# Kernel tuning notes

Measured on AMD Instinct MI355X. Metric: run time of the kernel, lower is better.

The kernel has to match this reference:

```python
import jax, jax.numpy as jnp
import numpy as np

N_NODES = 100000
D_IN = 128
H_DIM = 128
N_EDGES = 1600000


def _gcn_conv(x, src, dst, dinv, W, b):
    # PyG GCNConv(improved=True): h = x @ W; out = A_hat h + b,
    # A_hat = D^{-1/2} (A + 2I) D^{-1/2}
    h = x @ W                                   # [N, H]
    norm = dinv[src] * dinv[dst]                # [E]
    agg = jnp.zeros_like(h).at[dst].add(h[src] * norm[:, None])
    agg = agg + h * (2.0 * dinv * dinv)[:, None]  # self-loop, weight 2.0
    return agg + b


def setup_inputs() -> dict:
    key = jax.random.key(0)
    ks = jax.random.split(key, 12)
    s = 1.0 / np.sqrt(D_IN)
    sh = 1.0 / np.sqrt(2 * H_DIM)
    inp = {
        "x": jax.random.normal(ks[0], (N_NODES, D_IN), jnp.float32),
        "edge_index": jax.random.randint(ks[1], (2, N_EDGES), 0, N_NODES, jnp.int64),
        # GCNConv weights (in -> hidden), bias
        "Wz": jax.random.uniform(ks[2], (D_IN, H_DIM), jnp.float32, -s, s),
        "bz": jnp.zeros((H_DIM,), jnp.float32),
        "Wr": jax.random.uniform(ks[3], (D_IN, H_DIM), jnp.float32, -s, s),
        "br": jnp.zeros((H_DIM,), jnp.float32),
        "Wh": jax.random.uniform(ks[4], (D_IN, H_DIM), jnp.float32, -s, s),
        "bh": jnp.zeros((H_DIM,), jnp.float32),
        # TGCN gate linears: Linear(2h, h)
        "lzW": jax.random.uniform(ks[5], (2 * H_DIM, H_DIM), jnp.float32, -sh, sh),
        "lzb": jax.random.uniform(ks[6], (H_DIM,), jnp.float32, -sh, sh),
        "lrW": jax.random.uniform(ks[7], (2 * H_DIM, H_DIM), jnp.float32, -sh, sh),
        "lrb": jax.random.uniform(ks[8], (H_DIM,), jnp.float32, -sh, sh),
        "lhW": jax.random.uniform(ks[9], (2 * H_DIM, H_DIM), jnp.float32, -sh, sh),
        "lhb": jax.random.uniform(ks[10], (H_DIM,), jnp.float32, -sh, sh),
        # final linear2: hidden -> 1
        "W2": jax.random.uniform(ks[11], (H_DIM, 1), jnp.float32, -1 / np.sqrt(H_DIM), 1 / np.sqrt(H_DIM)),
        "b2": jnp.zeros((1,), jnp.float32),
    }
    return inp


def reference(x, edge_index, Wz, bz, Wr, br, Wh, bh, lzW, lzb, lrW, lrb, lhW, lhb, W2, b2):
    src, dst = edge_index[0], edge_index[1]
    n = x.shape[0]
    # improved GCN norm: deg includes self-loop weight 2
    deg = jnp.zeros((n,), x.dtype).at[dst].add(jnp.ones_like(src, x.dtype)) + 2.0
    dinv = jnp.where(deg > 0, deg ** -0.5, 0.0)
    # TGCN cell with H0 = 0
    H0 = jnp.zeros((n, Wz.shape[1]), x.dtype)
    Z = jax.nn.sigmoid(jnp.concatenate([_gcn_conv(x, src, dst, dinv, Wz, bz), H0], axis=1) @ lzW + lzb)
    R = jax.nn.sigmoid(jnp.concatenate([_gcn_conv(x, src, dst, dinv, Wr, br), H0], axis=1) @ lrW + lrb)
    Ht = jnp.tanh(jnp.concatenate([_gcn_conv(x, src, dst, dinv, Wh, bh), H0 * R], axis=1) @ lhW + lhb)
    H = Z * H0 + (1.0 - Z) * Ht
    # forward: relu output is discarded (y = h overwrites), then linear2
    return H @ W2 + b2
```

## Files before the change

### kernel.cpp

```cpp
#include <hip/hip_runtime.h>
#include <math.h>

#define D 128
#define BSHIFT 9
#define NB 196
#define EPT 7
#define P1B 241
#define CAPB 80
#define PSTRIDE (P1B * CAPB)
#define ECAP 9216
#define XCB4 782
#define PRB 32

typedef __attribute__((ext_vector_type(8))) short s8v;
typedef __attribute__((ext_vector_type(8))) unsigned short us8;
typedef __attribute__((ext_vector_type(4))) unsigned short us4;
typedef __attribute__((ext_vector_type(4))) float f4v;

__device__ __forceinline__ float bf2f(unsigned short u) {
    union { unsigned int i; float f; } v; v.i = ((unsigned int)u) << 16; return v.f;
}
__device__ __forceinline__ unsigned short f2bf(float f) {
    union { float f; unsigned int i; } v; v.f = f;
    unsigned int r = v.i + 0x7FFFu + ((v.i >> 16) & 1u);
    return (unsigned short)(r >> 16);
}

__global__ __launch_bounds__(1024) void k_pre(
    const int* __restrict__ src, const int* __restrict__ dst, int E,
    unsigned int* __restrict__ pairs, int* __restrict__ runlen,
    const float* __restrict__ x, unsigned short* __restrict__ xb, int n4,
    const float* __restrict__ Wz, const float* __restrict__ bz,
    const float* __restrict__ lzW, const float* __restrict__ lzb,
    const float* __restrict__ Wh, const float* __restrict__ bh,
    const float* __restrict__ lhW, const float* __restrict__ lhb,
    unsigned short* __restrict__ Mt, float* __restrict__ c) {
    __shared__ int cnt[256];
    __shared__ int loff[256];
    __shared__ unsigned int stage[EPT * 1024];
    int bx = blockIdx.x, tid = threadIdx.x;

    if (bx < P1B) {
        unsigned int pk[EPT]; int rkbk[EPT];
        int e0 = bx * (EPT * 1024) + tid;
        if (tid < 256) cnt[tid] = 0;
        __syncthreads();
        #pragma unroll
        for (int i = 0; i < EPT; ++i) {
            int e = e0 + i * 1024;
            bool ok = e < E;
            int d = ok ? dst[e] : 0;
            int s = ok ? src[e] : 0;
            int bk = d >> BSHIFT;
            pk[i] = ((unsigned int)(d & ((1 << BSHIFT) - 1)) << 17) | (unsigned int)s;
            int r = ok ? atomicAdd(&cnt[bk], 1) : 0;
            rkbk[i] = ok ? ((bk << 16) | r) : -1;
        }
        __syncthreads();
        if (tid < 64) {
            int v0 = cnt[tid * 4], v1 = cnt[tid * 4 + 1], v2 = cnt[tid * 4 + 2], v3 = cnt[tid * 4 + 3];
            int s = v0 + v1 + v2 + v3;
            int sc = s;
            #pragma unroll
            for (int off = 1; off < 64; off <<= 1) {
                int o = __shfl_up(sc, off, 64);
                if (tid >= off) sc += o;
            }
            int excl = sc - s;
            loff[tid * 4]     = excl;
            loff[tid * 4 + 1] = excl + v0;
            loff[tid * 4 + 2] = excl + v0 + v1;
            loff[tid * 4 + 3] = excl + v0 + v1 + v2;
        }
        __syncthreads();
        #pragma unroll
        for (int i = 0; i < EPT; ++i) {
            if (rkbk[i] >= 0) {
                int bk = rkbk[i] >> 16;
                stage[loff[bk] + (rkbk[i] & 0xffff)] = pk[i];
            }
        }
        if (tid < 256) runlen[bx * 256 + tid] = cnt[tid];
        __syncthreads();
        int wv = tid >> 6, lane = tid & 63;
        for (int b = wv; b < 256; b += 16) {
            int len = cnt[b];
            if (len == 0) continue;
            int lo = loff[b];
            unsigned int gbase = (unsigned int)b * PSTRIDE + (unsigned int)bx * CAPB;
            for (int j = lane; j < len; j += 64)
                pairs[gbase + j] = stage[lo + j];
        }
    } else if (bx < P1B + XCB4) {
        int i0 = (bx - P1B) * 4096 + tid;
        #pragma unroll
        for (int u = 0; u < 4; ++u) {
            int i = i0 + u * 1024;
            if (i < n4) {
                float4 v = ((const float4*)x)[i];
                us4 o;
                o[0] = f2bf(v.x); o[1] = f2bf(v.y); o[2] = f2bf(v.z); o[3] = f2bf(v.w);
                ((us4*)xb)[i] = o;
            }
        }
    } else {
        int k = (bx - (P1B + XCB4)) * 4 + (tid >> 8);
        int j = tid & 255;
        int jj = j & 127;
        const float* W = (j < 128) ? Wz : Wh;
        const float* L = (j < 128) ? lzW : lhW;
        float s = 0.f;
        for (int t = 0; t < 128; ++t) s += W[k * 128 + t] * L[t * 128 + jj];
        Mt[(size_t)j * 128 + k] = f2bf(s);
        if (k == 0) {
            const float* b  = (j < 128) ? bz  : bh;
            const float* lb = (j < 128) ? lzb : lhb;
            float cs = lb[jj];
            for (int t = 0; t < 128; ++t) cs += b[t] * L[t * 128 + jj];
            c[j] = cs;
        }
    }
}

__global__ __launch_bounds__(1024) void k_part2(
    const unsigned int* __restrict__ pairs, const int* __restrict__ runlen,
    int N,
    int* __restrict__ rowptr, int* __restrict__ deg, float* __restrict__ dinv,
    int* __restrict__ esrc) {
    __shared__ int cnt2[512];
    __shared__ int lcur[512];
    __shared__ int rl[256];
    __shared__ int sstage[ECAP];
    __shared__ int stot;
    int b = blockIdx.x, tid = threadIdx.x;
    int n0 = b << BSHIFT;
    int nn = min(N - n0, 1 << BSHIFT);
    long pb = (long)b * PSTRIDE;
    int wv = tid >> 6, lane = tid & 63;

    if (tid < 256) rl[tid] = (tid < P1B) ? runlen[tid * 256 + b] : 0;
    if (tid < 512) cnt2[tid] = 0;
    __syncthreads();
    for (int r = wv; r < P1B; r += 16) {
        int len = rl[r];
        long rb = pb + r * CAPB;
        for (int j = lane; j < len; j += 64)
            atomicAdd(&cnt2[pairs[rb + j] >> 17], 1);
    }
    __syncthreads();
    if (tid < 64) {
        int v[8]; int s = 0;
        #pragma unroll
        for (int k = 0; k < 8; ++k) { v[k] = cnt2[tid * 8 + k]; s += v[k]; }
        int sc = s;
        #pragma unroll
        for (int off = 1; off < 64; off <<= 1) {
            int o = __shfl_up(sc, off, 64);
            if (tid >= off) sc += o;
        }
        int excl = sc - s;
        if (tid == 63) stot = sc;
        #pragma unroll
        for (int k = 0; k < 8; ++k) {
            int node = tid * 8 + k;
            lcur[node] = excl;
            if (node < nn) {
                rowptr[n0 + node] = b * ECAP + excl;
                deg[n0 + node]    = v[k];
                dinv[n0 + node]   = rsqrtf((float)v[k] + 2.0f);
            }
            excl += v[k];
        }
    }
    __syncthreads();
    for (int r = wv; r < P1B; r += 16) {
        int len = rl[r];
        long rb = pb + r * CAPB;
        for (int j = lane; j < len; j += 64) {
            unsigned int p = pairs[rb + j];
            int pos = atomicAdd(&lcur[p >> 17], 1);
            sstage[pos] = (int)(p & 0x1FFFFu);
        }
    }
    __syncthreads();
    int tot = stot;
    for (int i = tid; i < tot; i += 1024)
        esrc[b * ECAP + i] = sstage[i];
}

__global__ __launch_bounds__(256) void k_gather(const unsigned short* __restrict__ xb,
                                                const int* __restrict__ esrc,
                                                const int* __restrict__ rowptr,
                                                const int* __restrict__ deg,
                                                const float* __restrict__ dinv,
                                                unsigned short* __restrict__ xab, int N) {
    int node = (blockIdx.x * blockDim.x + threadIdx.x) >> 5;
    int sub  = threadIdx.x & 31;
    if (node >= N) return;
    int eo = sub >> 4, cs = sub & 15;
    int start = rowptr[node];
    int end = start + deg[node];
    float dd = dinv[node];
    float acc[8];
    #pragma unroll
    for (int j = 0; j < 8; ++j) acc[j] = 0.f;

    for (int base = start; base < end; base += 32) {
        int cnt = min(32, end - base);
        int myedge = 0; float mynorm = 0.f;
        if (sub < cnt) { myedge = esrc[base + sub]; mynorm = dinv[myedge]; }
        int pairs = (cnt + 1) >> 1;
        int i = 0;
        for (; i + 3 < pairs; i += 4) {
            int i0 = 2 * i + eo;
            int   s0 = __shfl(myedge, i0,     32); float w0 = __shfl(mynorm, i0,     32);
            int   s1 = __shfl(myedge, i0 + 2, 32); float w1 = __shfl(mynorm, i0 + 2, 32);
            int   s2 = __shfl(myedge, i0 + 4, 32); float w2 = __shfl(mynorm, i0 + 4, 32);
            int   s3 = __shfl(myedge, i0 + 6, 32); float w3 = __shfl(mynorm, i0 + 6, 32);
            us8 v0 = *(const us8*)(xb + (size_t)s0 * D + cs * 8);
            us8 v1 = *(const us8*)(xb + (size_t)s1 * D + cs * 8);
            us8 v2 = *(const us8*)(xb + (size_t)s2 * D + cs * 8);
            us8 v3 = *(const us8*)(xb + (size_t)s3 * D + cs * 8);
            #pragma unroll
            for (int j = 0; j < 8; ++j) acc[j] += bf2f(v0[j]) * w0;
            #pragma unroll
            for (int j = 0; j < 8; ++j) acc[j] += bf2f(v1[j]) * w1;
            #pragma unroll
            for (int j = 0; j < 8; ++j) acc[j] += bf2f(v2[j]) * w2;
            #pragma unroll
            for (int j = 0; j < 8; ++j) acc[j] += bf2f(v3[j]) * w3;
        }
        for (; i < pairs; ++i) {
            int i0 = 2 * i + eo;
            int   s0 = __shfl(myedge, i0, 32); float w0 = __shfl(mynorm, i0, 32);
            us8 v0 = *(const us8*)(xb + (size_t)s0 * D + cs * 8);
            #pragma unroll
            for (int j = 0; j < 8; ++j) acc[j] += bf2f(v0[j]) * w0;
        }
    }
    #pragma unroll
    for (int j = 0; j < 8; ++j) acc[j] += __shfl_xor(acc[j], 16);
    if (eo == 0) {
        us8 xs = *(const us8*)(xb + (size_t)node * D + cs * 8);
        float sfac = 2.f * dd * dd;
        us8 r;
        #pragma unroll
        for (int j = 0; j < 8; ++j) r[j] = f2bf(acc[j] * dd + bf2f(xs[j]) * sfac);
        *(us8*)(xab + (size_t)node * D + cs * 8) = r;
    }
}

#define ASTRIDE 136
__global__ __launch_bounds__(256, 4) void k_ep_mfma(
    const unsigned short* __restrict__ xab, const unsigned short* __restrict__ Mt,
    const float* __restrict__ c, const float* __restrict__ W2,
    const float* __restrict__ b2, float* __restrict__ out, int N) {
    __shared__ unsigned short Ast[64 * ASTRIDE];
    __shared__ float pbuf[4][64];

    int tid = threadIdx.x;
    int n0 = blockIdx.x * 64;
    int wv = tid >> 6;
    int lane = tid & 63;
    int l = lane & 15, q = lane >> 4;

    #pragma unroll
    for (int j = 0; j < 4; ++j) {
        int idx = tid + 256 * j;
        int row = idx >> 4, c16 = idx & 15;
        us8 v = {0, 0, 0, 0, 0, 0, 0, 0};
        if (n0 + row < N) v = *(const us8*)(xab + (size_t)(n0 + row) * D + c16 * 8);
        *(us8*)&Ast[row * ASTRIDE + c16 * 8] = v;
    }
    __syncthreads();

    int tz0 = 2 * wv;
    f4v acc[4][4];
    #pragma unroll
    for (int i = 0; i < 4; ++i)
        #pragma unroll
        for (int nt = 0; nt < 4; ++nt) acc[i][nt] = (f4v){0.f, 0.f, 0.f, 0.f};

    const unsigned short* Bb = Mt + (size_t)l * 128 + q * 8;

    #pragma unroll
    for (int ks = 0; ks < 4; ++ks) {
        s8v b[4];
        #pragma unroll
        for (int i = 0; i < 2; ++i) {
            b[i]     = *(const s8v*)(Bb + (size_t)(tz0 + i) * 16 * 128 + ks * 32);
            b[2 + i] = *(const s8v*)(Bb + (size_t)(8 + tz0 + i) * 16 * 128 + ks * 32);
        }
        #pragma unroll
        for (int nt = 0; nt < 4; ++nt) {
            s8v a = *(const s8v*)&Ast[(nt * 16 + l) * ASTRIDE + ks * 32 + q * 8];
            #pragma unroll
            for (int i = 0; i < 4; ++i)
                acc[i][nt] = __builtin_amdgcn_mfma_f32_16x16x32_bf16(a, b[i], acc[i][nt], 0, 0, 0);
        }
    }

    float p[4][4];
    #pragma unroll
    for (int nt = 0; nt < 4; ++nt)
        #pragma unroll
        for (int r = 0; r < 4; ++r) p[nt][r] = 0.f;
    #pragma unroll
    for (int i = 0; i < 2; ++i) {
        int col = (tz0 + i) * 16 + l;
        float cz = c[col], ch = c[128 + col], w2 = W2[col];
        #pragma unroll
        for (int nt = 0; nt < 4; ++nt)
            #pragma unroll
            for (int r = 0; r < 4; ++r) {
                float gz = acc[i][nt][r] + cz;
                float gh = acc[2 + i][nt][r] + ch;
                float z  = 1.f / (1.f + __expf(-gz));
                float ht = 1.f - 2.f / (__expf(2.f * gh) + 1.f);
                p[nt][r] += (1.f - z) * ht * w2;
            }
    }
    #pragma unroll
    for (int nt = 0; nt < 4; ++nt)
        #pragma unroll
        for (int r = 0; r < 4; ++r) {
            p[nt][r] += __shfl_xor(p[nt][r], 1);
            p[nt][r] += __shfl_xor(p[nt][r], 2);
            p[nt][r] += __shfl_xor(p[nt][r], 4);
            p[nt][r] += __shfl_xor(p[nt][r], 8);
        }
    if (l == 0) {
        #pragma unroll
        for (int nt = 0; nt < 4; ++nt)
            #pragma unroll
            for (int r = 0; r < 4; ++r)
                pbuf[wv][nt * 16 + q * 4 + r] = p[nt][r];
    }
    __syncthreads();
    if (tid < 64) {
        int n = n0 + tid;
        if (n < N)
            out[n] = pbuf[0][tid] + pbuf[1][tid] + pbuf[2][tid] + pbuf[3][tid] + b2[0];
    }
}

extern "C" void kernel_launch(void* const* d_in, const int* in_sizes, int n_in,
                              void* d_out, int out_size, void* d_ws, size_t ws_size,
                              hipStream_t stream) {
    const float* x    = (const float*)d_in[0];
    const int*   eidx = (const int*)d_in[1];
    const float* Wz   = (const float*)d_in[2];
    const float* bz   = (const float*)d_in[3];
    const float* Wh   = (const float*)d_in[6];
    const float* bh   = (const float*)d_in[7];
    const float* lzW  = (const float*)d_in[8];
    const float* lzb  = (const float*)d_in[9];
    const float* lhW  = (const float*)d_in[12];
    const float* lhb  = (const float*)d_in[13];
    const float* W2   = (const float*)d_in[14];
    const float* b2   = (const float*)d_in[15];
    float* out = (float*)d_out;

    int N = in_sizes[0] / D;
    int E = in_sizes[1] / 2;
    const int* src = eidx;
    const int* dst = eidx + E;

    char* ws = (char*)d_ws;
    size_t off = 0;
    auto alloc = [&](size_t bytes) { void* p = ws + off; off += (bytes + 511) & ~(size_t)511; return p; };
    unsigned short* xb  = (unsigned short*)alloc((size_t)N * D * 2);
    unsigned short* xab = (unsigned short*)alloc((size_t)N * D * 2);
    int*   rowptr = (int*)  alloc((size_t)N * 4);
    int*   deg    = (int*)  alloc((size_t)N * 4);
    float* dinv   = (float*)alloc((size_t)N * 4);
    int*   esrc   = (int*)  alloc((size_t)NB * ECAP * 4);
    int*   runlen = (int*)  alloc((size_t)P1B * 256 * 4);
    unsigned short* Mt = (unsigned short*)alloc(256 * 128 * 2);
    float* c      = (float*)alloc(256 * 4);
    unsigned int* pairs = (unsigned int*)xab;

    int n4 = N * (D / 4);
    k_pre<<<P1B + XCB4 + PRB, 1024, 0, stream>>>(
        src, dst, E, pairs, runlen,
        x, xb, n4, Wz, bz, lzW, lzb, Wh, bh, lhW, lhb, Mt, c);
    k_part2<<<NB, 1024, 0, stream>>>(pairs, runlen, N, rowptr, deg, dinv, esrc);
    k_gather<<<(N * 32 + 255) / 256, 256, 0, stream>>>(xb, esrc, rowptr, deg, dinv, xab, N);
    k_ep_mfma<<<(N + 63) / 64, 256, 0, stream>>>(xab, Mt, c, W2, b2, out, N);
}
```

Measured before the change: 231.4 us.

## Compact bucket pair storage with global atomic cursors instead of fixed-capacity runs

Each first-pass block now reserves space in its destination bucket through a per-bucket global atomicAdd, so pairs are stored contiguously in a buffer of ECAP entries per bucket rather than in fixed 80-slot runs per source block. The second pass then reads one dense range per bucket with every thread striding over it, instead of walking 241 variable-length runs wave by wave. This removes the run-length array and the underused, poorly balanced loops over runs. It adds a memset and global atomics, and it makes the order of edges within a bucket nondeterministic.

```diff
diff --git a/kernel.cpp b/kernel.cpp
--- a/kernel.cpp
+++ b/kernel.cpp
@@ -6,8 +6,6 @@
 #define NB 196
 #define EPT 7
 #define P1B 241
-#define CAPB 80
-#define PSTRIDE (P1B * CAPB)
 #define ECAP 9216
 #define XCB4 782
 #define PRB 32
@@ -28,7 +26,7 @@
 
 __global__ __launch_bounds__(1024) void k_pre(
     const int* __restrict__ src, const int* __restrict__ dst, int E,
-    unsigned int* __restrict__ pairs, int* __restrict__ runlen,
+    unsigned int* __restrict__ pairs, int* __restrict__ gcur,
     const float* __restrict__ x, unsigned short* __restrict__ xb, int n4,
     const float* __restrict__ Wz, const float* __restrict__ bz,
     const float* __restrict__ lzW, const float* __restrict__ lzb,
@@ -80,14 +78,16 @@
                 stage[loff[bk] + (rkbk[i] & 0xffff)] = pk[i];
             }
         }
-        if (tid < 256) runlen[bx * 256 + tid] = cnt[tid];
         __syncthreads();
         int wv = tid >> 6, lane = tid & 63;
         for (int b = wv; b < 256; b += 16) {
             int len = cnt[b];
             if (len == 0) continue;
             int lo = loff[b];
-            unsigned int gbase = (unsigned int)b * PSTRIDE + (unsigned int)bx * CAPB;
+            int base = 0;
+            if (lane == 0) base = atomicAdd(&gcur[b], len);
+            base = __shfl(base, 0, 64);
+            unsigned int gbase = (unsigned int)b * ECAP + (unsigned int)base;
             for (int j = lane; j < len; j += 64)
                 pairs[gbase + j] = stage[lo + j];
         }
@@ -123,30 +123,23 @@
 }
 
 __global__ __launch_bounds__(1024) void k_part2(
-    const unsigned int* __restrict__ pairs, const int* __restrict__ runlen,
+    const unsigned int* __restrict__ pairs, const int* __restrict__ gcur,
     int N,
     int* __restrict__ rowptr, int* __restrict__ deg, float* __restrict__ dinv,
     int* __restrict__ esrc) {
     __shared__ int cnt2[512];
     __shared__ int lcur[512];
-    __shared__ int rl[256];
     __shared__ int sstage[ECAP];
-    __shared__ int stot;
     int b = blockIdx.x, tid = threadIdx.x;
     int n0 = b << BSHIFT;
     int nn = min(N - n0, 1 << BSHIFT);
-    long pb = (long)b * PSTRIDE;
-    int wv = tid >> 6, lane = tid & 63;
-
-    if (tid < 256) rl[tid] = (tid < P1B) ? runlen[tid * 256 + b] : 0;
+    int tot = gcur[b];
+    unsigned int bb = (unsigned int)b * ECAP;
+
     if (tid < 512) cnt2[tid] = 0;
     __syncthreads();
-    for (int r = wv; r < P1B; r += 16) {
-        int len = rl[r];
-        long rb = pb + r * CAPB;
-        for (int j = lane; j < len; j += 64)
-            atomicAdd(&cnt2[pairs[rb + j] >> 17], 1);
-    }
+    for (int j = tid; j < tot; j += 1024)
+        atomicAdd(&cnt2[pairs[bb + j] >> 17], 1);
     __syncthreads();
     if (tid < 64) {
         int v[8]; int s = 0;
@@ -159,7 +152,6 @@
             if (tid >= off) sc += o;
         }
         int excl = sc - s;
-        if (tid == 63) stot = sc;
         #pragma unroll
         for (int k = 0; k < 8; ++k) {
             int node = tid * 8 + k;
@@ -173,19 +165,14 @@
         }
     }
     __syncthreads();
-    for (int r = wv; r < P1B; r += 16) {
-        int len = rl[r];
-        long rb = pb + r * CAPB;
-        for (int j = lane; j < len; j += 64) {
-            unsigned int p = pairs[rb + j];
-            int pos = atomicAdd(&lcur[p >> 17], 1);
-            sstage[pos] = (int)(p & 0x1FFFFu);
-        }
-    }
-    __syncthreads();
-    int tot = stot;
+    for (int j = tid; j < tot; j += 1024) {
+        unsigned int p = pairs[bb + j];
+        int pos = atomicAdd(&lcur[p >> 17], 1);
+        sstage[pos] = (int)(p & 0x1FFFFu);
+    }
+    __syncthreads();
     for (int i = tid; i < tot; i += 1024)
-        esrc[b * ECAP + i] = sstage[i];
+        esrc[bb + i] = sstage[i];
 }
 
 __global__ __launch_bounds__(256) void k_gather(const unsigned short* __restrict__ xb,
@@ -375,16 +362,17 @@
     int*   deg    = (int*)  alloc((size_t)N * 4);
     float* dinv   = (float*)alloc((size_t)N * 4);
     int*   esrc   = (int*)  alloc((size_t)NB * ECAP * 4);
-    int*   runlen = (int*)  alloc((size_t)P1B * 256 * 4);
     unsigned short* Mt = (unsigned short*)alloc(256 * 128 * 2);
     float* c      = (float*)alloc(256 * 4);
+    int*   gcur   = (int*)  alloc(256 * 4);
     unsigned int* pairs = (unsigned int*)xab;
 
     int n4 = N * (D / 4);
+    hipMemsetAsync(gcur, 0, 256 * sizeof(int), stream);
     k_pre<<<P1B + XCB4 + PRB, 1024, 0, stream>>>(
-        src, dst, E, pairs, runlen,
+        src, dst, E, pairs, gcur,
         x, xb, n4, Wz, bz, lzW, lzb, Wh, bh, lhW, lhb, Mt, c);
-    k_part2<<<NB, 1024, 0, stream>>>(pairs, runlen, N, rowptr, deg, dinv, esrc);
+    k_part2<<<NB, 1024, 0, stream>>>(pairs, gcur, N, rowptr, deg, dinv, esrc);
     k_gather<<<(N * 32 + 255) / 256, 256, 0, stream>>>(xb, esrc, rowptr, deg, dinv, xab, N);
     k_ep_mfma<<<(N + 63) / 64, 256, 0, stream>>>(xab, Mt, c, W2, b2, out, N);
 }
```

Result: slower. 403.2 us (+74.2%).

## Regroup preprocessing kernels, cache pairs in LDS, and double-tile the epilogue

Applied to the files above, without the earlier changes.

The x-to-bf16 conversion and the weight-folding blocks move out of the edge-partition kernel and into the second-stage kernel. They now run alongside the per-bucket CSR build instead of alongside the first edge pass. The second stage reads pairs from global memory once into an LDS raw buffer and does its scatter from LDS, where before it read global memory twice. Part1 writes pairs as uint2 pairs. The MFMA epilogue now handles two 64-row tiles per block and prefetches the second tile's rows into registers while the first is being computed. This is meant to hide load latency, at the cost of more registers and more LDS use, which can lower occupancy.

```diff
diff --git a/kernel.cpp b/kernel.cpp
--- a/kernel.cpp
+++ b/kernel.cpp
@@ -26,39 +26,102 @@
     return (unsigned short)(r >> 16);
 }
 
-__global__ __launch_bounds__(1024) void k_pre(
+__global__ __launch_bounds__(1024) void k_part1(
     const int* __restrict__ src, const int* __restrict__ dst, int E,
-    unsigned int* __restrict__ pairs, int* __restrict__ runlen,
+    unsigned int* __restrict__ pairs, int* __restrict__ runlen) {
+    __shared__ int cnt[256];
+    __shared__ int loff[256];
+    __shared__ unsigned int stage[EPT * 1024];
+    int bx = blockIdx.x, tid = threadIdx.x;
+
+    unsigned int pk[EPT]; int rkbk[EPT];
+    int e0 = bx * (EPT * 1024) + tid;
+    if (tid < 256) cnt[tid] = 0;
+    __syncthreads();
+    #pragma unroll
+    for (int i = 0; i < EPT; ++i) {
+        int e = e0 + i * 1024;
+        bool ok = e < E;
+        int d = ok ? dst[e] : 0;
+        int s = ok ? src[e] : 0;
+        int bk = d >> BSHIFT;
+        pk[i] = ((unsigned int)(d & ((1 << BSHIFT) - 1)) << 17) | (unsigned int)s;
+        int r = ok ? atomicAdd(&cnt[bk], 1) : 0;
+        rkbk[i] = ok ? ((bk << 16) | r) : -1;
+    }
+    __syncthreads();
+    if (tid < 64) {
+        int v0 = cnt[tid * 4], v1 = cnt[tid * 4 + 1], v2 = cnt[tid * 4 + 2], v3 = cnt[tid * 4 + 3];
+        int s = v0 + v1 + v2 + v3;
+        int sc = s;
+        #pragma unroll
+        for (int off = 1; off < 64; off <<= 1) {
+            int o = __shfl_up(sc, off, 64);
+            if (tid >= off) sc += o;
+        }
+        int excl = sc - s;
+        loff[tid * 4]     = excl;
+        loff[tid * 4 + 1] = excl + v0;
+        loff[tid * 4 + 2] = excl + v0 + v1;
+        loff[tid * 4 + 3] = excl + v0 + v1 + v2;
+    }
+    __syncthreads();
+    #pragma unroll
+    for (int i = 0; i < EPT; ++i) {
+        if (rkbk[i] >= 0) {
+            int bk = rkbk[i] >> 16;
+            stage[loff[bk] + (rkbk[i] & 0xffff)] = pk[i];
+        }
+    }
+    if (tid < 256) runlen[bx * 256 + tid] = cnt[tid];
+    __syncthreads();
+    int wv = tid >> 6, lane = tid & 63;
+    for (int b = wv; b < 256; b += 16) {
+        int len = cnt[b];
+        if (len == 0) continue;
+        int lo = loff[b];
+        unsigned int gbase = (unsigned int)b * PSTRIDE + (unsigned int)bx * CAPB;
+        for (int j = lane; 2 * j < len; j += 64) {
+            unsigned int a = stage[lo + 2 * j];
+            unsigned int bsec = (2 * j + 1 < len) ? stage[lo + 2 * j + 1] : 0u;
+            uint2 w; w.x = a; w.y = bsec;
+            *(uint2*)(pairs + gbase + 2 * j) = w;
+        }
+    }
+}
+
+__global__ __launch_bounds__(1024) void k_mid2(
+    const unsigned int* __restrict__ pairs, const int* __restrict__ runlen,
+    int N,
+    int* __restrict__ rowptr, int* __restrict__ deg, float* __restrict__ dinv,
+    int* __restrict__ esrc,
     const float* __restrict__ x, unsigned short* __restrict__ xb, int n4,
     const float* __restrict__ Wz, const float* __restrict__ bz,
     const float* __restrict__ lzW, const float* __restrict__ lzb,
     const float* __restrict__ Wh, const float* __restrict__ bh,
     const float* __restrict__ lhW, const float* __restrict__ lhb,
     unsigned short* __restrict__ Mt, float* __restrict__ c) {
-    __shared__ int cnt[256];
-    __shared__ int loff[256];
-    __shared__ unsigned int stage[EPT * 1024];
+    __shared__ int cnt2[512];
+    __shared__ int lcur[512];
+    __shared__ int rl[256];
+    __shared__ int runoff[256];
+    __shared__ int raw[ECAP];
+    __shared__ int sorted[ECAP];
+    __shared__ int stot;
     int bx = blockIdx.x, tid = threadIdx.x;
 
-    if (bx < P1B) {
-        unsigned int pk[EPT]; int rkbk[EPT];
-        int e0 = bx * (EPT * 1024) + tid;
-        if (tid < 256) cnt[tid] = 0;
-        __syncthreads();
-        #pragma unroll
-        for (int i = 0; i < EPT; ++i) {
-            int e = e0 + i * 1024;
-            bool ok = e < E;
-            int d = ok ? dst[e] : 0;
-            int s = ok ? src[e] : 0;
-            int bk = d >> BSHIFT;
-            pk[i] = ((unsigned int)(d & ((1 << BSHIFT) - 1)) << 17) | (unsigned int)s;
-            int r = ok ? atomicAdd(&cnt[bk], 1) : 0;
-            rkbk[i] = ok ? ((bk << 16) | r) : -1;
-        }
+    if (bx < NB) {
+        int b = bx;
+        int n0 = b << BSHIFT;
+        int nn = min(N - n0, 1 << BSHIFT);
+        long pb = (long)b * PSTRIDE;
+        int wv = tid >> 6, lane = tid & 63;
+
+        if (tid < 256) rl[tid] = (tid < P1B) ? runlen[tid * 256 + b] : 0;
+        if (tid < 512) cnt2[tid] = 0;
         __syncthreads();
         if (tid < 64) {
-            int v0 = cnt[tid * 4], v1 = cnt[tid * 4 + 1], v2 = cnt[tid * 4 + 2], v3 = cnt[tid * 4 + 3];
+            int v0 = rl[tid * 4], v1 = rl[tid * 4 + 1], v2 = rl[tid * 4 + 2], v3 = rl[tid * 4 + 3];
             int s = v0 + v1 + v2 + v3;
             int sc = s;
             #pragma unroll
@@ -67,32 +130,59 @@
                 if (tid >= off) sc += o;
             }
             int excl = sc - s;
-            loff[tid * 4]     = excl;
-            loff[tid * 4 + 1] = excl + v0;
-            loff[tid * 4 + 2] = excl + v0 + v1;
-            loff[tid * 4 + 3] = excl + v0 + v1 + v2;
-        }
-        __syncthreads();
-        #pragma unroll
-        for (int i = 0; i < EPT; ++i) {
-            if (rkbk[i] >= 0) {
-                int bk = rkbk[i] >> 16;
-                stage[loff[bk] + (rkbk[i] & 0xffff)] = pk[i];
-            }
-        }
-        if (tid < 256) runlen[bx * 256 + tid] = cnt[tid];
-        __syncthreads();
-        int wv = tid >> 6, lane = tid & 63;
-        for (int b = wv; b < 256; b += 16) {
-            int len = cnt[b];
-            if (len == 0) continue;
-            int lo = loff[b];
-            unsigned int gbase = (unsigned int)b * PSTRIDE + (unsigned int)bx * CAPB;
-            for (int j = lane; j < len; j += 64)
-                pairs[gbase + j] = stage[lo + j];
-        }
-    } else if (bx < P1B + XCB4) {
-        int i0 = (bx - P1B) * 4096 + tid;
+            if (tid == 63) stot = sc;
+            runoff[tid * 4]     = excl;
+            runoff[tid * 4 + 1] = excl + v0;
+            runoff[tid * 4 + 2] = excl + v0 + v1;
+            runoff[tid * 4 + 3] = excl + v0 + v1 + v2;
+        }
+        __syncthreads();
+        for (int r = wv; r < P1B; r += 16) {
+            int len = rl[r];
+            int ro = runoff[r];
+            long rb = pb + r * CAPB;
+            for (int j = lane; j < len; j += 64) {
+                unsigned int p = pairs[rb + j];
+                raw[ro + j] = (int)p;
+                atomicAdd(&cnt2[p >> 17], 1);
+            }
+        }
+        __syncthreads();
+        if (tid < 64) {
+            int v[8]; int s = 0;
+            #pragma unroll
+            for (int k = 0; k < 8; ++k) { v[k] = cnt2[tid * 8 + k]; s += v[k]; }
+            int sc = s;
+            #pragma unroll
+            for (int off = 1; off < 64; off <<= 1) {
+                int o = __shfl_up(sc, off, 64);
+                if (tid >= off) sc += o;
+            }
+            int excl = sc - s;
+            #pragma unroll
+            for (int k = 0; k < 8; ++k) {
+                int node = tid * 8 + k;
+                lcur[node] = excl;
+                if (node < nn) {
+                    rowptr[n0 + node] = b * ECAP + excl;
+                    deg[n0 + node]    = v[k];
+                    dinv[n0 + node]   = rsqrtf((float)v[k] + 2.0f);
+                }
+                excl += v[k];
+            }
+        }
+        __syncthreads();
+        int tot = stot;
+        for (int i = tid; i < tot; i += 1024) {
+            unsigned int p = (unsigned int)raw[i];
+            int pos = atomicAdd(&lcur[p >> 17], 1);
+            sorted[pos] = (int)(p & 0x1FFFFu);
+        }
+        __syncthreads();
+        for (int i = tid; i < tot; i += 1024)
+            esrc[b * ECAP + i] = sorted[i];
+    } else if (bx < NB + XCB4) {
+        int i0 = (bx - NB) * 4096 + tid;
         #pragma unroll
         for (int u = 0; u < 4; ++u) {
             int i = i0 + u * 1024;
@@ -104,7 +194,7 @@
             }
         }
     } else {
-        int k = (bx - (P1B + XCB4)) * 4 + (tid >> 8);
+        int k = (bx - (NB + XCB4)) * 4 + (tid >> 8);
         int j = tid & 255;
         int jj = j & 127;
         const float* W = (j < 128) ? Wz : Wh;
@@ -120,72 +210,6 @@
             c[j] = cs;
         }
     }
-}
-
-__global__ __launch_bounds__(1024) void k_part2(
-    const unsigned int* __restrict__ pairs, const int* __restrict__ runlen,
-    int N,
-    int* __restrict__ rowptr, int* __restrict__ deg, float* __restrict__ dinv,
-    int* __restrict__ esrc) {
-    __shared__ int cnt2[512];
-    __shared__ int lcur[512];
-    __shared__ int rl[256];
-    __shared__ int sstage[ECAP];
-    __shared__ int stot;
-    int b = blockIdx.x, tid = threadIdx.x;
-    int n0 = b << BSHIFT;
-    int nn = min(N - n0, 1 << BSHIFT);
-    long pb = (long)b * PSTRIDE;
-    int wv = tid >> 6, lane = tid & 63;
-
-    if (tid < 256) rl[tid] = (tid < P1B) ? runlen[tid * 256 + b] : 0;
-    if (tid < 512) cnt2[tid] = 0;
-    __syncthreads();
-    for (int r = wv; r < P1B; r += 16) {
-        int len = rl[r];
-        long rb = pb + r * CAPB;
-        for (int j = lane; j < len; j += 64)
-            atomicAdd(&cnt2[pairs[rb + j] >> 17], 1);
-    }
-    __syncthreads();
-    if (tid < 64) {
-        int v[8]; int s = 0;
-        #pragma unroll
-        for (int k = 0; k < 8; ++k) { v[k] = cnt2[tid * 8 + k]; s += v[k]; }
-        int sc = s;
-        #pragma unroll
-        for (int off = 1; off < 64; off <<= 1) {
-            int o = __shfl_up(sc, off, 64);
-            if (tid >= off) sc += o;
-        }
-        int excl = sc - s;
-        if (tid == 63) stot = sc;
-        #pragma unroll
-        for (int k = 0; k < 8; ++k) {
-            int node = tid * 8 + k;
-            lcur[node] = excl;
-            if (node < nn) {
-                rowptr[n0 + node] = b * ECAP + excl;
-                deg[n0 + node]    = v[k];
-                dinv[n0 + node]   = rsqrtf((float)v[k] + 2.0f);
-            }
-            excl += v[k];
-        }
-    }
-    __syncthreads();
-    for (int r = wv; r < P1B; r += 16) {
-        int len = rl[r];
-        long rb = pb + r * CAPB;
-        for (int j = lane; j < len; j += 64) {
-            unsigned int p = pairs[rb + j];
-            int pos = atomicAdd(&lcur[p >> 17], 1);
-            sstage[pos] = (int)(p & 0x1FFFFu);
-        }
-    }
-    __syncthreads();
-    int tot = stot;
-    for (int i = tid; i < tot; i += 1024)
-        esrc[b * ECAP + i] = sstage[i];
 }
 
 __global__ __launch_bounds__(256) void k_gather(const unsigned short* __restrict__ xb,
@@ -259,88 +283,117 @@
     __shared__ float pbuf[4][64];
 
     int tid = threadIdx.x;
-    int n0 = blockIdx.x * 64;
     int wv = tid >> 6;
     int lane = tid & 63;
     int l = lane & 15, q = lane >> 4;
+    int tz0 = 2 * wv;
+    const unsigned short* Bb = Mt + (size_t)l * 128 + q * 8;
+    int ldrow = tid >> 4, ldc = tid & 15;
+
+    us8 v0[4], v1[4];
+    int t0 = blockIdx.x * 128;
+    int t1 = t0 + 64;
 
     #pragma unroll
     for (int j = 0; j < 4; ++j) {
         int idx = tid + 256 * j;
         int row = idx >> 4, c16 = idx & 15;
-        us8 v = {0, 0, 0, 0, 0, 0, 0, 0};
-        if (n0 + row < N) v = *(const us8*)(xab + (size_t)(n0 + row) * D + c16 * 8);
-        *(us8*)&Ast[row * ASTRIDE + c16 * 8] = v;
+        us8 z = {0, 0, 0, 0, 0, 0, 0, 0};
+        v0[j] = (t0 + row < N) ? *(const us8*)(xab + (size_t)(t0 + row) * D + c16 * 8) : z;
+    }
+    #pragma unroll
+    for (int j = 0; j < 4; ++j) {
+        int idx = tid + 256 * j;
+        int row = idx >> 4, c16 = idx & 15;
+        *(us8*)&Ast[row * ASTRIDE + c16 * 8] = v0[j];
     }
     __syncthreads();
-
-    int tz0 = 2 * wv;
-    f4v acc[4][4];
-    #pragma unroll
-    for (int i = 0; i < 4; ++i)
-        #pragma unroll
-        for (int nt = 0; nt < 4; ++nt) acc[i][nt] = (f4v){0.f, 0.f, 0.f, 0.f};
-
-    const unsigned short* Bb = Mt + (size_t)l * 128 + q * 8;
-
-    #pragma unroll
-    for (int ks = 0; ks < 4; ++ks) {
-        s8v b[4];
+    #pragma unroll
+    for (int j = 0; j < 4; ++j) {
+        int idx = tid + 256 * j;
+        int row = idx >> 4, c16 = idx & 15;
+        us8 z = {0, 0, 0, 0, 0, 0, 0, 0};
+        v1[j] = (t1 + row < N) ? *(const us8*)(xab + (size_t)(t1 + row) * D + c16 * 8) : z;
+    }
+
+    #pragma unroll
+    for (int tile = 0; tile < 2; ++tile) {
+        int n0 = tile ? t1 : t0;
+        f4v acc[4][4];
+        #pragma unroll
+        for (int i = 0; i < 4; ++i)
+            #pragma unroll
+            for (int nt = 0; nt < 4; ++nt) acc[i][nt] = (f4v){0.f, 0.f, 0.f, 0.f};
+
+        #pragma unroll
+        for (int ks = 0; ks < 4; ++ks) {
+            s8v b[4];
+            #pragma unroll
+            for (int i = 0; i < 2; ++i) {
+                b[i]     = *(const s8v*)(Bb + (size_t)(tz0 + i) * 16 * 128 + ks * 32);
+                b[2 + i] = *(const s8v*)(Bb + (size_t)(8 + tz0 + i) * 16 * 128 + ks * 32);
+            }
+            #pragma unroll
+            for (int nt = 0; nt < 4; ++nt) {
+                s8v a = *(const s8v*)&Ast[(nt * 16 + l) * ASTRIDE + ks * 32 + q * 8];
+                #pragma unroll
+                for (int i = 0; i < 4; ++i)
+                    acc[i][nt] = __builtin_amdgcn_mfma_f32_16x16x32_bf16(a, b[i], acc[i][nt], 0, 0, 0);
+            }
+        }
+
+        float p[4][4];
+        #pragma unroll
+        for (int nt = 0; nt < 4; ++nt)
+            #pragma unroll
+            for (int r = 0; r < 4; ++r) p[nt][r] = 0.f;
         #pragma unroll
         for (int i = 0; i < 2; ++i) {
-            b[i]     = *(const s8v*)(Bb + (size_t)(tz0 + i) * 16 * 128 + ks * 32);
-            b[2 + i] = *(const s8v*)(Bb + (size_t)(8 + tz0 + i) * 16 * 128 + ks * 32);
-        }
-        #pragma unroll
-        for (int nt = 0; nt < 4; ++nt) {
-            s8v a = *(const s8v*)&Ast[(nt * 16 + l) * ASTRIDE + ks * 32 + q * 8];
-            #pragma unroll
-            for (int i = 0; i < 4; ++i)
-                acc[i][nt] = __builtin_amdgcn_mfma_f32_16x16x32_bf16(a, b[i], acc[i][nt], 0, 0, 0);
-        }
-    }
-
-    float p[4][4];
-    #pragma unroll
-    for (int nt = 0; nt < 4; ++nt)
-        #pragma unroll
-        for (int r = 0; r < 4; ++r) p[nt][r] = 0.f;
-    #pragma unroll
-    for (int i = 0; i < 2; ++i) {
-        int col = (tz0 + i) * 16 + l;
-        float cz = c[col], ch = c[128 + col], w2 = W2[col];
+            int col = (tz0 + i) * 16 + l;
+            float cz = c[col], ch = c[128 + col], w2 = W2[col];
+            #pragma unroll
+            for (int nt = 0; nt < 4; ++nt)
+                #pragma unroll
+                for (int r = 0; r < 4; ++r) {
+                    float gz = acc[i][nt][r] + cz;
+                    float gh = acc[2 + i][nt][r] + ch;
+                    float z  = 1.f / (1.f + __expf(-gz));
+                    float ht = 1.f - 2.f / (__expf(2.f * gh) + 1.f);
+                    p[nt][r] += (1.f - z) * ht * w2;
+                }
+        }
         #pragma unroll
         for (int nt = 0; nt < 4; ++nt)
             #pragma unroll
             for (int r = 0; r < 4; ++r) {
-                float gz = acc[i][nt][r] + cz;
-                float gh = acc[2 + i][nt][r] + ch;
-                float z  = 1.f / (1.f + __expf(-gz));
-                float ht = 1.f - 2.f / (__expf(2.f * gh) + 1.f);
-                p[nt][r] += (1.f - z) * ht * w2;
-            }
-    }
-    #pragma unroll
-    for (int nt = 0; nt < 4; ++nt)
-        #pragma unroll
-        for (int r = 0; r < 4; ++r) {
-            p[nt][r] += __shfl_xor(p[nt][r], 1);
-            p[nt][r] += __shfl_xor(p[nt][r], 2);
-            p[nt][r] += __shfl_xor(p[nt][r], 4);
-            p[nt][r] += __shfl_xor(p[nt][r], 8);
-        }
-    if (l == 0) {
-        #pragma unroll
-        for (int nt = 0; nt < 4; ++nt)
-            #pragma unroll
-            for (int r = 0; r < 4; ++r)
-                pbuf[wv][nt * 16 + q * 4 + r] = p[nt][r];
-    }
-    __syncthreads();
-    if (tid < 64) {
-        int n = n0 + tid;
-        if (n < N)
-            out[n] = pbuf[0][tid] + pbuf[1][tid] + pbuf[2][tid] + pbuf[3][tid] + b2[0];
+                p[nt][r] += __shfl_xor(p[nt][r], 1);
+                p[nt][r] += __shfl_xor(p[nt][r], 2);
+                p[nt][r] += __shfl_xor(p[nt][r], 4);
+                p[nt][r] += __shfl_xor(p[nt][r], 8);
+            }
+        if (l == 0) {
+            #pragma unroll
+            for (int nt = 0; nt < 4; ++nt)
+                #pragma unroll
+                for (int r = 0; r < 4; ++r)
+                    pbuf[wv][nt * 16 + q * 4 + r] = p[nt][r];
+        }
+        __syncthreads();
+        if (tid < 64) {
+            int n = n0 + tid;
+            if (n < N)
+                out[n] = pbuf[0][tid] + pbuf[1][tid] + pbuf[2][tid] + pbuf[3][tid] + b2[0];
+        }
+        if (tile == 0) {
+            __syncthreads();
+            #pragma unroll
+            for (int j = 0; j < 4; ++j) {
+                int idx = tid + 256 * j;
+                int row = idx >> 4, c16 = idx & 15;
+                *(us8*)&Ast[row * ASTRIDE + c16 * 8] = v1[j];
+            }
+            __syncthreads();
+        }
     }
 }
 
@@ -381,10 +434,10 @@
     unsigned int* pairs = (unsigned int*)xab;
 
     int n4 = N * (D / 4);
-    k_pre<<<P1B + XCB4 + PRB, 1024, 0, stream>>>(
-        src, dst, E, pairs, runlen,
+    k_part1<<<P1B, 1024, 0, stream>>>(src, dst, E, pairs, runlen);
+    k_mid2<<<NB + XCB4 + PRB, 1024, 0, stream>>>(
+        pairs, runlen, N, rowptr, deg, dinv, esrc,
         x, xb, n4, Wz, bz, lzW, lzb, Wh, bh, lhW, lhb, Mt, c);
-    k_part2<<<NB, 1024, 0, stream>>>(pairs, runlen, N, rowptr, deg, dinv, esrc);
     k_gather<<<(N * 32 + 255) / 256, 256, 0, stream>>>(xb, esrc, rowptr, deg, dinv, xab, N);
-    k_ep_mfma<<<(N + 63) / 64, 256, 0, stream>>>(xab, Mt, c, W2, b2, out, N);
-}
+    k_ep_mfma<<<(N + 127) / 128, 256, 0, stream>>>(xab, Mt, c, W2, b2, out, N);
+}
```

Result: slower. 238.8 us (+3.2%).

## Stage bucketed edge pairs in LDS once, vectorize pair stores, split gather launch

Applied to the files above, without the earlier changes.

The node-bucketing kernel now reads each block's edge pairs from global memory only once. It copies them into an LDS buffer at per-run offsets and counts degrees in the same pass. The counting sort then scatters from that LDS copy into a second LDS array, instead of re-reading the pairs from global memory. The first kernel writes its staged pairs as 64-bit uint2 stores, zero-padding an odd tail. The gather kernel is launched as two halves over the node range, which adds a launch and doubles LDS use in the partition kernel, which may reduce occupancy.

```diff
diff --git a/kernel.cpp b/kernel.cpp
--- a/kernel.cpp
+++ b/kernel.cpp
@@ -88,8 +88,12 @@
             if (len == 0) continue;
             int lo = loff[b];
             unsigned int gbase = (unsigned int)b * PSTRIDE + (unsigned int)bx * CAPB;
-            for (int j = lane; j < len; j += 64)
-                pairs[gbase + j] = stage[lo + j];
+            for (int j = lane; 2 * j < len; j += 64) {
+                unsigned int a = stage[lo + 2 * j];
+                unsigned int bsec = (2 * j + 1 < len) ? stage[lo + 2 * j + 1] : 0u;
+                uint2 w; w.x = a; w.y = bsec;
+                *(uint2*)(pairs + gbase + 2 * j) = w;
+            }
         }
     } else if (bx < P1B + XCB4) {
         int i0 = (bx - P1B) * 4096 + tid;
@@ -122,7 +126,7 @@
     }
 }
 
-__global__ __launch_bounds__(1024) void k_part2(
+__global__ __launch_bounds__(1024) void k_p2(
     const unsigned int* __restrict__ pairs, const int* __restrict__ runlen,
     int N,
     int* __restrict__ rowptr, int* __restrict__ deg, float* __restrict__ dinv,
@@ -130,7 +134,9 @@
     __shared__ int cnt2[512];
     __shared__ int lcur[512];
     __shared__ int rl[256];
-    __shared__ int sstage[ECAP];
+    __shared__ int runoff[256];
+    __shared__ int raw[ECAP];
+    __shared__ int sorted[ECAP];
     __shared__ int stot;
     int b = blockIdx.x, tid = threadIdx.x;
     int n0 = b << BSHIFT;
@@ -141,17 +147,9 @@
     if (tid < 256) rl[tid] = (tid < P1B) ? runlen[tid * 256 + b] : 0;
     if (tid < 512) cnt2[tid] = 0;
     __syncthreads();
-    for (int r = wv; r < P1B; r += 16) {
-        int len = rl[r];
-        long rb = pb + r * CAPB;
-        for (int j = lane; j < len; j += 64)
-            atomicAdd(&cnt2[pairs[rb + j] >> 17], 1);
-    }
-    __syncthreads();
     if (tid < 64) {
-        int v[8]; int s = 0;
-        #pragma unroll
-        for (int k = 0; k < 8; ++k) { v[k] = cnt2[tid * 8 + k]; s += v[k]; }
+        int v0 = rl[tid * 4], v1 = rl[tid * 4 + 1], v2 = rl[tid * 4 + 2], v3 = rl[tid * 4 + 3];
+        int s = v0 + v1 + v2 + v3;
         int sc = s;
         #pragma unroll
         for (int off = 1; off < 64; off <<= 1) {
@@ -160,6 +158,34 @@
         }
         int excl = sc - s;
         if (tid == 63) stot = sc;
+        runoff[tid * 4]     = excl;
+        runoff[tid * 4 + 1] = excl + v0;
+        runoff[tid * 4 + 2] = excl + v0 + v1;
+        runoff[tid * 4 + 3] = excl + v0 + v1 + v2;
+    }
+    __syncthreads();
+    for (int r = wv; r < P1B; r += 16) {
+        int len = rl[r];
+        int ro = runoff[r];
+        long rb = pb + r * CAPB;
+        for (int j = lane; j < len; j += 64) {
+            unsigned int p = pairs[rb + j];
+            raw[ro + j] = (int)p;
+            atomicAdd(&cnt2[p >> 17], 1);
+        }
+    }
+    __syncthreads();
+    if (tid < 64) {
+        int v[8]; int s = 0;
+        #pragma unroll
+        for (int k = 0; k < 8; ++k) { v[k] = cnt2[tid * 8 + k]; s += v[k]; }
+        int sc = s;
+        #pragma unroll
+        for (int off = 1; off < 64; off <<= 1) {
+            int o = __shfl_up(sc, off, 64);
+            if (tid >= off) sc += o;
+        }
+        int excl = sc - s;
         #pragma unroll
         for (int k = 0; k < 8; ++k) {
             int node = tid * 8 + k;
@@ -173,19 +199,15 @@
         }
     }
     __syncthreads();
-    for (int r = wv; r < P1B; r += 16) {
-        int len = rl[r];
-        long rb = pb + r * CAPB;
-        for (int j = lane; j < len; j += 64) {
-            unsigned int p = pairs[rb + j];
-            int pos = atomicAdd(&lcur[p >> 17], 1);
-            sstage[pos] = (int)(p & 0x1FFFFu);
-        }
-    }
-    __syncthreads();
     int tot = stot;
+    for (int i = tid; i < tot; i += 1024) {
+        unsigned int p = (unsigned int)raw[i];
+        int pos = atomicAdd(&lcur[p >> 17], 1);
+        sorted[pos] = (int)(p & 0x1FFFFu);
+    }
+    __syncthreads();
     for (int i = tid; i < tot; i += 1024)
-        esrc[b * ECAP + i] = sstage[i];
+        esrc[b * ECAP + i] = sorted[i];
 }
 
 __global__ __launch_bounds__(256) void k_gather(const unsigned short* __restrict__ xb,
@@ -193,10 +215,11 @@
                                                 const int* __restrict__ rowptr,
                                                 const int* __restrict__ deg,
                                                 const float* __restrict__ dinv,
-                                                unsigned short* __restrict__ xab, int N) {
-    int node = (blockIdx.x * blockDim.x + threadIdx.x) >> 5;
+                                                unsigned short* __restrict__ xab,
+                                                int n_off, int n_end) {
+    int node = ((blockIdx.x * blockDim.x + threadIdx.x) >> 5) + n_off;
     int sub  = threadIdx.x & 31;
-    if (node >= N) return;
+    if (node >= n_end) return;
     int eo = sub >> 4, cs = sub & 15;
     int start = rowptr[node];
     int end = start + deg[node];
@@ -384,7 +407,9 @@
     k_pre<<<P1B + XCB4 + PRB, 1024, 0, stream>>>(
         src, dst, E, pairs, runlen,
         x, xb, n4, Wz, bz, lzW, lzb, Wh, bh, lhW, lhb, Mt, c);
-    k_part2<<<NB, 1024, 0, stream>>>(pairs, runlen, N, rowptr, deg, dinv, esrc);
-    k_gather<<<(N * 32 + 255) / 256, 256, 0, stream>>>(xb, esrc, rowptr, deg, dinv, xab, N);
+    k_p2<<<NB, 1024, 0, stream>>>(pairs, runlen, N, rowptr, deg, dinv, esrc);
+    int half = (N + 1) / 2;
+    k_gather<<<(half * 32 + 255) / 256, 256, 0, stream>>>(xb, esrc, rowptr, deg, dinv, xab, 0, half);
+    k_gather<<<((N - half) * 32 + 255) / 256, 256, 0, stream>>>(xb, esrc, rowptr, deg, dinv, xab, half, N);
     k_ep_mfma<<<(N + 63) / 64, 256, 0, stream>>>(xab, Mt, c, W2, b2, out, N);
 }
```

Measured after the change: 238.1 us. 2.9% more time.
